# Kernel optimization log

Measured on AMD Instinct MI355X. Metric: run time of the kernel, lower is better.

Reference implementation:

```python
import jax, jax.numpy as jnp
import numpy as np

DN = ('NCHW', 'OIHW', 'NCHW')


def conv(x, w, s, p):
    return jax.lax.conv_general_dilated(x, w, (s, s), [(p, p), (p, p)], dimension_numbers=DN)


def batchnorm(x, g, b, eps=1e-5):
    # torch BatchNorm2d in training mode: biased batch stats over (N,H,W)
    mu = jnp.mean(x, (0, 2, 3), keepdims=True)
    var = jnp.var(x, (0, 2, 3), keepdims=True)
    return (x - mu) * jax.lax.rsqrt(var + eps) * g.reshape(1, -1, 1, 1) + b.reshape(1, -1, 1, 1)


def pconv(x, mask, W, b, s, p, gb, act):
    # PartialConvLayer.forward
    k = W.shape[-1]
    y = conv(x * mask, W, s, p)
    mc = conv(mask, jnp.ones((1, 1, k, k), x.dtype), s, p)  # all-ones mask conv (frozen)
    zero = mc == 0
    msum = jnp.where(zero, 1.0, mc)
    if b is not None:
        bias = b.reshape(1, -1, 1, 1)
        y = (y - bias) / msum + bias
    else:
        y = y / msum
    y = jnp.where(zero, 0.0, y)
    new_mask = jnp.where(zero, 0.0, 1.0).astype(x.dtype)
    if gb is not None:
        y = batchnorm(y, gb[0], gb[1])
    if act == 'relu':
        y = jax.nn.relu(y)
    elif act == 'leaky':
        y = jnp.where(y >= 0, y, 0.2 * y)
    return y, new_mask


def nlm(mask, feat, h2):
    # Vectorized batch_NLM: Nadaraya-Watson estimator between miss and bkg pixels.
    # Equivalent to the original triple loop: for each miss pixel i,
    #   out[i] = sum_j exp(-||x_i-x_j||^2/h^2) x_j / sum_j exp(-...)   over bkg j.
    # Subtracting the per-row min distance before exp is mathematically identical
    # (the factor cancels in the ratio) and numerically stable.
    bs, C, H, W = feat.shape
    N = H * W
    x = feat.transpose(0, 2, 3, 1).reshape(bs, N, C)
    bkg = mask.reshape(bs, N) > 0.5
    sq = jnp.sum(x * x, -1)  # [bs,N]
    D = jnp.maximum(sq[:, :, None] + sq[:, None, :] - 2.0 * jnp.einsum('bic,bjc->bij', x, x), 0.0)
    Dm = jnp.where(bkg[:, None, :], D, jnp.inf)
    dmin = jnp.min(Dm, -1, keepdims=True)
    w = jnp.where(bkg[:, None, :], jnp.exp(-(D - dmin) / h2), 0.0)
    avg = jnp.einsum('bij,bjc->bic', w, x) / jnp.sum(w, -1, keepdims=True)
    out = jnp.where(bkg[:, :, None], x, avg)  # only miss pixels are replaced
    return out.reshape(bs, H, W, C).transpose(0, 3, 1, 2)


def up2(x):
    return jnp.repeat(jnp.repeat(x, 2, axis=2), 2, axis=3)


def forward(input_x, mask, enc1_W, enc2_W, enc3_W, enc4_W, dec4_W, dec3_W, dec2_W, dec1_W, dec1_b,
            enc2_g, enc2_b, enc3_g, enc3_b, enc4_g, enc4_b,
            dec4_g, dec4_b, dec3_g, dec3_b, dec2_g, dec2_b):
    H_GAUSS2 = 25.0  # h_gaussian = 5
    h0, m0 = input_x, mask
    h1, m1 = pconv(h0, m0, enc1_W, None, 2, 3, None, 'relu')                 # down-7, bn=False
    h2, m2 = pconv(h1, m1, enc2_W, None, 2, 2, (enc2_g, enc2_b), 'relu')     # down-5
    # NLM feature swapping at layer 2 (torch code detaches -> stop_gradient)
    h2 = jax.lax.stop_gradient(nlm(m2, h2, H_GAUSS2))
    buffer_swapped = h2
    h3, m3 = pconv(h2, m2, enc3_W, None, 2, 1, (enc3_g, enc3_b), 'relu')     # down-3
    h4, m4 = pconv(h3, m3, enc4_W, None, 2, 1, (enc4_g, enc4_b), 'relu')     # down-3

    out, omask = h4, m4
    out, omask = up2(out), up2(omask)
    out, omask = pconv(jnp.concatenate([out, h3], 1), omask, dec4_W, None, 1, 1, (dec4_g, dec4_b), 'leaky')
    out, omask = up2(out), up2(omask)
    out, omask = pconv(jnp.concatenate([out, buffer_swapped], 1), omask, dec3_W, None, 1, 1, (dec3_g, dec3_b), 'leaky')
    out, omask = up2(out), up2(omask)
    out, omask = pconv(jnp.concatenate([out, h1], 1), omask, dec2_W, None, 1, 1, (dec2_g, dec2_b), 'leaky')
    out, omask = up2(out), up2(omask)
    out, omask = pconv(jnp.concatenate([out, h0], 1), omask, dec1_W, dec1_b, 1, 1, None, 'none')  # bn=False, bias, no act
    return out


def setup_inputs() -> dict:
    key = jax.random.key(0)
    ks = jax.random.split(key, 12)

    def kaiming(k, shape):
        fan_in = shape[1] * shape[2] * shape[3]
        return jax.random.normal(k, shape, jnp.float32) * np.float32(np.sqrt(2.0 / fan_in))

    bs = 8
    input_x = jax.random.normal(ks[0], (bs, 128, 144, 144), jnp.float32)
    # mask: 1 = background (valid), 0 = missing. Hole large enough to survive two downsamples.
    mask = jnp.ones((bs, 1, 144, 144), jnp.float32).at[:, :, 40:96, 40:96].set(0.0)

    inp = {
        'input_x': input_x,
        'mask': mask,
        'enc1_W': kaiming(ks[1], (256, 128, 7, 7)),
        'enc2_W': kaiming(ks[2], (512, 256, 5, 5)),
        'enc3_W': kaiming(ks[3], (512, 512, 3, 3)),
        'enc4_W': kaiming(ks[4], (512, 512, 3, 3)),
        'dec4_W': kaiming(ks[5], (512, 1024, 3, 3)),
        'dec3_W': kaiming(ks[6], (512, 1024, 3, 3)),
        'dec2_W': kaiming(ks[7], (256, 768, 3, 3)),
        'dec1_W': kaiming(ks[8], (128, 384, 3, 3)),
        'dec1_b': jnp.zeros((128,), jnp.float32),
    }
    for name, c in [('enc2', 512), ('enc3', 512), ('enc4', 512), ('dec4', 512), ('dec3', 512), ('dec2', 256)]:
        inp[name + '_g'] = jnp.ones((c,), jnp.float32)
        inp[name + '_b'] = jnp.zeros((c,), jnp.float32)
    return inp


def reference(input_x, mask, enc1_W, enc2_W, enc3_W, enc4_W, dec4_W, dec3_W, dec2_W, dec1_W, dec1_b,
              enc2_g, enc2_b, enc3_g, enc3_b, enc4_g, enc4_b,
              dec4_g, dec4_b, dec3_g, dec3_b, dec2_g, dec2_b):
    return forward(input_x, mask, enc1_W, enc2_W, enc3_W, enc4_W, dec4_W, dec3_W, dec2_W, dec1_W, dec1_b,
                   enc2_g, enc2_b, enc3_g, enc3_b, enc4_g, enc4_b,
                   dec4_g, dec4_b, dec3_g, dec3_b, dec2_g, dec2_b)
```

## Files before the change

### kernel.cpp

```cpp
#include <hip/hip_runtime.h>
#include <math.h>

#define ACT_NONE 0
#define ACT_RELU 1
#define ACT_LEAKY 2

#define EPI_F32 0
#define EPI_PAIR_RELU 1
#define EPI_F32_BIAS 2

typedef __attribute__((ext_vector_type(8))) short short8;
typedef __attribute__((ext_vector_type(8))) __bf16 bf16x8;
typedef __attribute__((ext_vector_type(4))) float f32x4;
typedef __attribute__((ext_vector_type(4))) unsigned uint4v;

__device__ __forceinline__ float actf(float y, int act) {
    if (act == ACT_RELU)  return y > 0.f ? y : 0.f;
    if (act == ACT_LEAKY) return y >= 0.f ? y : 0.2f * y;
    return y;
}

__device__ __forceinline__ unsigned f2bf_rne(float f) {
    unsigned u = __float_as_uint(f);
    return (u + 0x7FFFu + ((u >> 16) & 1u)) >> 16;
}
__device__ __forceinline__ float bf2f(unsigned h) { return __uint_as_float(h << 16); }
__device__ __forceinline__ unsigned splitpack(float f) {
    unsigned hi = f2bf_rne(f);
    float r = f - bf2f(hi);
    unsigned lo = f2bf_rne(r);
    return (hi & 0xFFFFu) | (lo << 16);
}

__device__ __forceinline__ f32x4 mfma16(short8 a, short8 b, f32x4 c) {
    return __builtin_amdgcn_mfma_f32_16x16x32_bf16(
        __builtin_bit_cast(bf16x8, a), __builtin_bit_cast(bf16x8, b), c, 0, 0, 0);
}

__device__ __forceinline__ size_t paddr(int img, int KBc, size_t HW, size_t pix) {
    return ((size_t)img * KBc * HW + pix) * 32;
}

template<int K, int S, bool MHALF>
__global__ void maskconv_kernel(const float* __restrict__ M, int HM, int WM,
                                float* __restrict__ mc, float* __restrict__ nm,
                                int N, int Hin, int Win, int Hout, int Wout) {
    constexpr int P = (K - 1) / 2;
    int idx = blockIdx.x * blockDim.x + threadIdx.x;
    int total = N * Hout * Wout;
    if (idx >= total) return;
    int wo = idx % Wout;
    int t  = idx / Wout;
    int ho = t % Hout;
    int n  = t / Hout;
    float s = 0.f;
    for (int kh = 0; kh < K; ++kh) {
        int ih = ho * S - P + kh;
        if ((unsigned)ih >= (unsigned)Hin) continue;
        const float* mrow = M + ((size_t)n * HM + (MHALF ? (ih >> 1) : ih)) * WM;
        for (int kw = 0; kw < K; ++kw) {
            int iw = wo * S - P + kw;
            if ((unsigned)iw < (unsigned)Win)
                s += mrow[MHALF ? (iw >> 1) : iw];
        }
    }
    mc[idx] = s;
    nm[idx] = (s == 0.f) ? 0.f : 1.f;
}

__global__ void wtransform(const float* __restrict__ W, short* __restrict__ Whi,
                           short* __restrict__ Wlo, int Cout, int Cin, int Ksz,
                           size_t total) {
    size_t idx = (size_t)blockIdx.x * blockDim.x + threadIdx.x;
    if (idx >= total) return;
    int j = (int)(idx & 7);
    int lane = (int)((idx >> 3) & 63);
    size_t r = idx >> 9;
    int COB = Cout >> 4, KB = Cin >> 5;
    int cob = (int)(r % COB); r /= COB;
    int kb = (int)(r % KB);
    int tap = (int)(r / KB);
    int co = cob * 16 + (lane & 15);
    int ci = kb * 32 + (lane >> 4) * 8 + j;
    float f = W[((size_t)co * Cin + ci) * Ksz + tap];
    unsigned hi = f2bf_rne(f);
    float rr = f - bf2f(hi);
    unsigned lo = f2bf_rne(rr);
    Whi[idx] = (short)hi;
    Wlo[idx] = (short)lo;
}

template<int K, int S, int TH, int TW, int NFW, bool AF32, int EPI>
__global__ __launch_bounds__(512) void conv_enc(
    const void* __restrict__ Ahi, const void* __restrict__ Alo,
    int Cin, int Hin, int Win,
    const float* __restrict__ M,
    const short* __restrict__ Whi, const short* __restrict__ Wlo,
    const float* __restrict__ mc, const float* __restrict__ bias,
    void* __restrict__ outp, void* __restrict__ outp2,
    int Hout, int Wout, int Cout, int TX)
{
    static_assert(S == 2, "parity layout assumes stride 2");
    constexpr int P = (K - 1) / 2;
    constexpr int HH  = (TH - 1) * S + K;
    constexpr int HWC = (TW - 1) * S + K;
    constexpr int PXC = HH * HWC;
    static_assert(PXC <= 512, "one halo pixel per thread");
    constexpr int PW  = (HWC + 1) / 2;
    constexpr int PXC2 = HH * PW * 2;
    constexpr int PXC2P = PXC2 + ((2 - (PXC2 % 8) + 8) % 8);
    __shared__ __align__(16) short BHs[4 * PXC2P * 8];
    __shared__ __align__(16) short BLs[4 * PXC2P * 8];

    const int t    = threadIdx.x;
    const int lane = t & 63;
    const int wv   = t >> 6;
    const int wm   = wv >> 1;
    const int wn   = wv & 1;
    const int img  = blockIdx.z;
    const int coB  = blockIdx.y * 256;
    const int tile = blockIdx.x;
    const int ty   = tile / TX, tx = tile - ty * TX;
    const int oy0  = ty * TH, ox0 = tx * TW;
    const int KB   = Cin >> 5;
    const int COB  = Cout >> 4;
    const size_t HW = (size_t)Hin * Win;
    const int g  = lane >> 4;
    const int pl = lane & 15;

    bool sel = false;
    size_t basef = 0, basep = 0;
    int qq = 0;
    if (t < PXC) {
        const int r = t / HWC, c = t - r * HWC;
        qq = r * PW + (c >> 1) + (c & 1) * (HH * PW);
        const int iy = oy0 * S - P + r;
        const int ix = ox0 * S - P + c;
        if ((unsigned)iy < (unsigned)Hin && (unsigned)ix < (unsigned)Win) {
            const size_t pix = (size_t)iy * Win + ix;
            if (M[(size_t)img * HW + pix] != 0.f) {
                sel = true;
                basef = (size_t)img * Cin * HW + pix;
                basep = paddr(img, KB, HW, pix);
            }
        }
    }

    short8 hv[4], lv[4];
    auto prefetch = [&](int kb) {
#pragma unroll
        for (int gg = 0; gg < 4; ++gg) {
            if (sel) {
                if (AF32) {
                    const float* s = (const float*)Ahi + basef + (size_t)(kb * 32 + gg * 8) * HW;
#pragma unroll
                    for (int j = 0; j < 8; ++j) {
                        float f = s[(size_t)j * HW];
                        unsigned h16 = f2bf_rne(f);
                        float rr = f - bf2f(h16);
                        hv[gg][j] = (short)h16;
                        lv[gg][j] = (short)f2bf_rne(rr);
                    }
                } else {
                    const size_t a = basep + (size_t)kb * HW * 32 + gg * 8;
                    hv[gg] = *(const short8*)((const short*)Ahi + a);
                    lv[gg] = *(const short8*)((const short*)Alo + a);
                }
            } else {
#pragma unroll
                for (int j = 0; j < 8; ++j) { hv[gg][j] = 0; lv[gg][j] = 0; }
            }
        }
    };

    f32x4 acc[4][NFW] = {};
    if (t < PXC) prefetch(0);

#pragma unroll 1
    for (int kb = 0; kb < KB; ++kb) {
        if (t < PXC) {
#pragma unroll
            for (int gg = 0; gg < 4; ++gg) {
                *(short8*)&BHs[(gg * PXC2P + qq) * 8] = hv[gg];
                *(short8*)&BLs[(gg * PXC2P + qq) * 8] = lv[gg];
            }
        }
        __syncthreads();
        if (t < PXC && kb + 1 < KB) prefetch(kb + 1);

#pragma unroll 1
        for (int kh = 0; kh < K; ++kh)
#pragma unroll 1
        for (int kw = 0; kw < K; ++kw) {
            const int tap = kh * K + kw;
            const size_t wb = (((size_t)tap * KB + kb) * COB + (coB >> 4) + wm * 4) * 512
                            + (size_t)lane * 8;
            short8 ah[4], al[4];
#pragma unroll
            for (int fm = 0; fm < 4; ++fm) {
                ah[fm] = *(const short8*)(Whi + wb + (size_t)fm * 512);
                al[fm] = *(const short8*)(Wlo + wb + (size_t)fm * 512);
            }
#pragma unroll
            for (int fn = 0; fn < NFW; ++fn) {
                const int pxf = (wn * NFW + fn) * 16 + pl;
                const int oy = pxf / TW, ox = pxf - oy * TW;
                const int q2 = (oy * S + kh) * PW + ox + (kw >> 1) + (kw & 1) * (HH * PW);
                short8 bh = *(const short8*)&BHs[(g * PXC2P + q2) * 8];
                short8 bl = *(const short8*)&BLs[(g * PXC2P + q2) * 8];
#pragma unroll
                for (int fm = 0; fm < 4; ++fm) {
                    acc[fm][fn] = mfma16(ah[fm], bh, acc[fm][fn]);
                    acc[fm][fn] = mfma16(al[fm], bh, acc[fm][fn]);
                    acc[fm][fn] = mfma16(ah[fm], bl, acc[fm][fn]);
                }
            }
        }
        __syncthreads();
    }

    const int Npix = Hout * Wout;
    const float* mcb = mc + (size_t)img * Npix;
#pragma unroll
    for (int fm = 0; fm < 4; ++fm)
#pragma unroll
    for (int fn = 0; fn < NFW; ++fn) {
        const int co = coB + (wm * 4 + fm) * 16 + (lane >> 4) * 4;
        const int pxf = (wn * NFW + fn) * 16 + (lane & 15);
        const int oy = pxf / TW, ox = pxf - oy * TW;
        const int gy = oy0 + oy, gx = ox0 + ox;
        if (gy >= Hout || gx >= Wout) continue;
        const size_t pix = (size_t)gy * Wout + gx;
        const float m = mcb[pix];
        f32x4 a = acc[fm][fn];
#pragma unroll
        for (int r = 0; r < 4; ++r) {
            float y = a[r];
            if (EPI == EPI_F32_BIAS) {
                const float bv = bias[co + r];
                y = (m == 0.f) ? 0.f : (y - bv) / m + bv;
            } else {
                y = (m == 0.f) ? 0.f : y / m;
            }
            if (EPI == EPI_PAIR_RELU) {
                y = y > 0.f ? y : 0.f;
                const size_t pa = paddr(img, Cout >> 5, Npix, pix)
                                + (size_t)(co >> 5) * Npix * 32 + (co & 31) + r;
                unsigned h16 = f2bf_rne(y);
                float rr = y - bf2f(h16);
                ((short*)outp)[pa]  = (short)h16;
                ((short*)outp2)[pa] = (short)f2bf_rne(rr);
            } else {
                ((float*)outp)[((size_t)img * Cout + co + r) * Npix + pix] = y;
            }
        }
    }
}

template<int TH, int TW, int NFW, bool BF32, int EPI>
__global__ __launch_bounds__(512) void conv3x3(
    const void* __restrict__ Ahi, const void* __restrict__ Alo,
    int CA, int HA, int WA,
    const void* __restrict__ Bhi, const void* __restrict__ Blo, int CB,
    const float* __restrict__ M,
    const short* __restrict__ Whi, const short* __restrict__ Wlo,
    const float* __restrict__ mc, const float* __restrict__ bias,
    void* __restrict__ outp,
    int Hout, int Wout, int Cout, int TX)
{
    constexpr int HALO_H = TH + 2, HALO_W = TW + 2, HALO = HALO_H * HALO_W;
    constexpr int HALOP = HALO + ((2 - (HALO % 8) + 8) % 8);
    constexpr int NPIX = TH * TW;
    constexpr int SITER = (HALO + 127) / 128;
    static_assert(NPIX == 32 * NFW, "tile must be exactly 32*NFW pixels");
    __shared__ __align__(16) short BHs[4 * HALOP * 8];
    __shared__ __align__(16) short BLs[4 * HALOP * 8];

    const int t    = threadIdx.x;
    const int lane = t & 63;
    const int wv   = t >> 6;
    const int wm   = wv >> 1;
    const int wn   = wv & 1;
    const int img  = blockIdx.z;
    const int coB  = blockIdx.y * 128;
    const int tile = blockIdx.x;
    const int ty   = tile / TX;
    const int tx   = tile - ty * TX;
    const int oy0  = ty * TH, ox0 = tx * TW;
    const int Cin  = CA + CB;
    const int KB   = Cin >> 5;
    const int KBA  = CA >> 5;
    const int KBB  = CB >> 5;
    const int COB  = Cout >> 4;
    const int WM   = Wout >> 1;
    const size_t HWA = (size_t)HA * WA;
    const size_t HWB = (size_t)Hout * Wout;

    const int sg = t >> 7;
    const int st = t & 127;
    const int g  = lane >> 4;
    const int pl = lane & 15;

    bool ssel[SITER];
    size_t aoff[SITER], boff[SITER];
#pragma unroll
    for (int i = 0; i < SITER; ++i) {
        ssel[i] = false; aoff[i] = 0; boff[i] = 0;
        const int q = st + i * 128;
        if (q < HALO) {
            const int hy = q / HALO_W, hx = q - hy * HALO_W;
            const int iy = oy0 - 1 + hy, ix = ox0 - 1 + hx;
            if ((unsigned)iy < (unsigned)Hout && (unsigned)ix < (unsigned)Wout) {
                if (M[((size_t)img * (Hout >> 1) + (iy >> 1)) * WM + (ix >> 1)] != 0.f) {
                    ssel[i] = true;
                    const size_t pixA = (size_t)(iy >> 1) * WA + (ix >> 1);
                    const size_t pixB = (size_t)iy * Wout + ix;
                    aoff[i] = paddr(img, KBA, HWA, pixA) + sg * 8;
                    if (BF32) boff[i] = (size_t)img * CB * HWB + pixB;
                    else      boff[i] = paddr(img, KBB, HWB, pixB) + sg * 8;
                }
            }
        }
    }

    short8 hv[SITER], lv[SITER];
    auto prefetch = [&](int kb) {
        const int c = kb * 32 + sg * 8;
#pragma unroll
        for (int i = 0; i < SITER; ++i) {
            const int q = st + i * 128;
            bool ok = (q < HALO) && ssel[i];
            if (ok) {
                if (c < CA) {
                    const size_t a = aoff[i] + (size_t)kb * HWA * 32;
                    hv[i] = *(const short8*)((const short*)Ahi + a);
                    lv[i] = *(const short8*)((const short*)Alo + a);
                } else {
                    if (BF32) {
                        const float* s = (const float*)Bhi + boff[i] + (size_t)(c - CA) * HWB;
#pragma unroll
                        for (int j = 0; j < 8; ++j) {
                            float f = s[(size_t)j * HWB];
                            unsigned h16 = f2bf_rne(f);
                            float rr = f - bf2f(h16);
                            hv[i][j] = (short)h16;
                            lv[i][j] = (short)f2bf_rne(rr);
                        }
                    } else {
                        const size_t a = boff[i] + (size_t)(kb - KBA) * HWB * 32;
                        hv[i] = *(const short8*)((const short*)Bhi + a);
                        lv[i] = *(const short8*)((const short*)Blo + a);
                    }
                }
            } else {
#pragma unroll
                for (int j = 0; j < 8; ++j) { hv[i][j] = 0; lv[i][j] = 0; }
            }
        }
    };

    f32x4 acc[2][NFW] = {};
    const size_t wstride = (size_t)KB * COB * 512;
    prefetch(0);

#pragma unroll 1
    for (int kb = 0; kb < KB; ++kb) {
#pragma unroll
        for (int i = 0; i < SITER; ++i) {
            const int q = st + i * 128;
            if (q < HALO) {
                *(short8*)&BHs[(sg * HALOP + q) * 8] = hv[i];
                *(short8*)&BLs[(sg * HALOP + q) * 8] = lv[i];
            }
        }
        __syncthreads();
        if (kb + 1 < KB) prefetch(kb + 1);

        size_t wb = ((size_t)kb * COB + (coB >> 4) + wm * 2) * 512 + lane * 8;
#pragma unroll 1
        for (int tap = 0; tap < 9; ++tap) {
            const int dh = tap / 3, dw = tap - dh * 3;
            short8 ah0 = *(const short8*)(Whi + wb);
            short8 ah1 = *(const short8*)(Whi + wb + 512);
            short8 al0 = *(const short8*)(Wlo + wb);
            short8 al1 = *(const short8*)(Wlo + wb + 512);
#pragma unroll
            for (int fn = 0; fn < NFW; ++fn) {
                const int pxf = (wn * NFW + fn) * 16 + pl;
                const int oy = pxf / TW, ox = pxf - oy * TW;
                const int hpx = (oy + dh) * HALO_W + (ox + dw);
                short8 bh = *(const short8*)&BHs[(g * HALOP + hpx) * 8];
                short8 bl = *(const short8*)&BLs[(g * HALOP + hpx) * 8];
                acc[0][fn] = mfma16(ah0, bh, acc[0][fn]);
                acc[1][fn] = mfma16(ah1, bh, acc[1][fn]);
                acc[0][fn] = mfma16(al0, bh, acc[0][fn]);
                acc[1][fn] = mfma16(al1, bh, acc[1][fn]);
                acc[0][fn] = mfma16(ah0, bl, acc[0][fn]);
                acc[1][fn] = mfma16(ah1, bl, acc[1][fn]);
            }
            wb += wstride;
        }
        __syncthreads();
    }

    const float* mcb = mc + (size_t)img * HWB;
#pragma unroll
    for (int fm = 0; fm < 2; ++fm)
#pragma unroll
    for (int fn = 0; fn < NFW; ++fn) {
        const int co = coB + (wm * 2 + fm) * 16 + (lane >> 4) * 4;
        const int pxf = (wn * NFW + fn) * 16 + (lane & 15);
        const int oy = pxf / TW, ox = pxf - oy * TW;
        const int gy = oy0 + oy, gx = ox0 + ox;
        if (gy >= Hout || gx >= Wout) continue;
        const float m = mcb[(size_t)gy * Wout + gx];
        f32x4 a = acc[fm][fn];
#pragma unroll
        for (int r = 0; r < 4; ++r) {
            float y = a[r];
            if (EPI == EPI_F32_BIAS) {
                const float bv = bias[co + r];
                y = (m == 0.f) ? 0.f : (y - bv) / m + bv;
            } else {
                y = (m == 0.f) ? 0.f : y / m;
            }
            ((float*)outp)[((size_t)img * Cout + co + r) * HWB + (size_t)gy * Wout + gx] = y;
        }
    }
}

__global__ __launch_bounds__(256) void bn_stats_kernel(const float* __restrict__ y,
                                                       int N, int C, int HW,
                                                       float* __restrict__ mean,
                                                       float* __restrict__ istd) {
    const int c = blockIdx.x;
    double s = 0.0, s2 = 0.0;
    const int tot = N * HW;
    for (int i = threadIdx.x; i < tot; i += blockDim.x) {
        int n = i / HW, hw = i - n * HW;
        float v = y[((size_t)n * C + c) * HW + hw];
        s += v;
        s2 += (double)v * v;
    }
    __shared__ double sh[256], sh2[256];
    sh[threadIdx.x] = s; sh2[threadIdx.x] = s2;
    __syncthreads();
    for (int o = 128; o > 0; o >>= 1) {
        if (threadIdx.x < o) { sh[threadIdx.x] += sh[threadIdx.x + o]; sh2[threadIdx.x] += sh2[threadIdx.x + o]; }
        __syncthreads();
    }
    if (threadIdx.x == 0) {
        double mu = sh[0] / tot;
        double var = sh2[0] / tot - mu * mu;
        mean[c] = (float)mu;
        istd[c] = (float)(1.0 / sqrt(var + 1e-5));
    }
}

__global__ __launch_bounds__(256) void bn_apply_blk(
    const float* __restrict__ y,
    const float* __restrict__ mean, const float* __restrict__ istd,
    const float* __restrict__ g, const float* __restrict__ b,
    short* __restrict__ hi, short* __restrict__ lo, float* __restrict__ fout,
    int C, int HW, int act) {
    __shared__ float tile[32][65];
    const int img = blockIdx.z, kb = blockIdx.y;
    const int px0 = blockIdx.x * 64;
    const int tid = threadIdx.x;
    const int KBc = C >> 5;

    for (int i = tid; i < 32 * 64; i += 256) {
        const int ch = i >> 6, px = i & 63;
        float v = 0.f;
        if (px0 + px < HW)
            v = y[((size_t)img * C + kb * 32 + ch) * HW + px0 + px];
        tile[ch][px] = v;
    }
    __syncthreads();

    const int px = tid >> 2, sg = tid & 3;
    if (px0 + px < HW) {
        short8 h8, l8;
        float f8[8];
#pragma unroll
        for (int j = 0; j < 8; ++j) {
            const int c = kb * 32 + sg * 8 + j;
            float v = tile[sg * 8 + j][px];
            v = (v - mean[c]) * istd[c] * g[c] + b[c];
            v = actf(v, act);
            f8[j] = v;
            unsigned h16 = f2bf_rne(v);
            float rr = v - bf2f(h16);
            h8[j] = (short)h16;
            l8[j] = (short)f2bf_rne(rr);
        }
        const size_t a = (((size_t)img * KBc + kb) * HW + px0 + px) * 32 + sg * 8;
        *(short8*)&hi[a] = h8;
        *(short8*)&lo[a] = l8;
        if (fout) {
#pragma unroll
            for (int j = 0; j < 8; ++j)
                fout[((size_t)img * C + kb * 32 + sg * 8 + j) * HW + px0 + px] = f8[j];
        }
    }
}

#define NLM_C 512
#define NLM_N 1296
#define NLM_MAXM 256
#define NLM_RT 16
#define NLM_KB1 16
#define NLM_KB2 41
#define NLM_PFRAG (NLM_KB1 * NLM_RT * 512)
#define NLM_WFRAG (NLM_KB2 * NLM_RT * 512)

__global__ __launch_bounds__(256) void nlm_trans(const float* __restrict__ h2f,
                                                 unsigned* __restrict__ xTp) {
    __shared__ float tile[32][33];
    const int b = blockIdx.z;
    const int j0 = blockIdx.x * 32, c0 = blockIdx.y * 32;
    const int tx = threadIdx.x & 31, ty = threadIdx.x >> 5;
    for (int cc = ty; cc < 32; cc += 8) {
        const int j = j0 + tx;
        tile[cc][tx] = (j < NLM_N) ? h2f[((size_t)b * NLM_C + c0 + cc) * NLM_N + j] : 0.f;
    }
    __syncthreads();
    for (int jj = ty; jj < 32; jj += 8) {
        const int j = j0 + jj;
        if (j < NLM_N)
            xTp[((size_t)b * NLM_N + j) * NLM_C + c0 + tx] = splitpack(tile[tx][jj]);
    }
}

__global__ void nlm_sq2(const float* __restrict__ h2f, float* __restrict__ sq) {
    const int b = blockIdx.y;
    const int j = blockIdx.x * 256 + threadIdx.x;
    if (j >= NLM_N) return;
    const float* p = h2f + (size_t)b * NLM_C * NLM_N + j;
    float s0 = 0.f, s1 = 0.f, s2 = 0.f, s3 = 0.f;
    for (int c = 0; c < NLM_C; c += 4) {
        float v0 = p[(size_t)c * NLM_N];
        float v1 = p[(size_t)(c + 1) * NLM_N];
        float v2 = p[(size_t)(c + 2) * NLM_N];
        float v3 = p[(size_t)(c + 3) * NLM_N];
        s0 = fmaf(v0, v0, s0); s1 = fmaf(v1, v1, s1);
        s2 = fmaf(v2, v2, s2); s3 = fmaf(v3, v3, s3);
    }
    sq[b * NLM_N + j] = (s0 + s1) + (s2 + s3);
}

__global__ void nlm_compact(const float* __restrict__ nm2, int* __restrict__ list,
                            int* __restrict__ cnt) {
    const int b = blockIdx.x;
    for (int j = threadIdx.x; j < NLM_N; j += 256) {
        if (nm2[(size_t)b * NLM_N + j] == 0.f) {
            int pos = atomicAdd(&cnt[b], 1);
            if (pos < NLM_MAXM) list[b * NLM_MAXM + pos] = j;
        }
    }
}

__global__ void nlm_gather(const unsigned* __restrict__ xTp, const int* __restrict__ list,
                           const int* __restrict__ cnt,
                           short* __restrict__ Phi, short* __restrict__ Plo) {
    const int b = blockIdx.y;
    const int id = blockIdx.x * 256 + threadIdx.x;
    const int i  = id >> 6;
    const int rem = id & 63;
    const int kb = rem >> 2, kg = rem & 3;
    const int lane = kg * 16 + (i & 15), rt = i >> 4;
    const size_t f = (size_t)b * NLM_PFRAG + ((size_t)(kb * NLM_RT + rt) * 64 + lane) * 8;
    if (i < cnt[b]) {
        const int pix = list[b * NLM_MAXM + i];
        const unsigned* s = xTp + ((size_t)b * NLM_N + pix) * NLM_C + kb * 32 + kg * 8;
#pragma unroll
        for (int jj = 0; jj < 8; ++jj) {
            unsigned v = s[jj];
            Phi[f + jj] = (short)(v & 0xFFFFu);
            Plo[f + jj] = (short)(v >> 16);
        }
    } else {
#pragma unroll
        for (int jj = 0; jj < 8; ++jj) { Phi[f + jj] = 0; Plo[f + jj] = 0; }
    }
}

__global__ __launch_bounds__(512) void nlm_gemm1(
    const unsigned* __restrict__ xTp, const short* __restrict__ Phi,
    const short* __restrict__ Plo, const int* __restrict__ cnt,
    float* __restrict__ S) {
    const int img = blockIdx.z, mt = blockIdx.y, nt = blockIdx.x;
    if (mt * 128 >= cnt[img]) return;
    __shared__ __align__(16) unsigned BH[4 * 128 * 4];
    __shared__ __align__(16) unsigned BL[4 * 128 * 4];
    const int t = threadIdx.x, lane = t & 63, wv = t >> 6, wm = wv >> 1, wn = wv & 1;
    const int j0 = nt * 128;
    const int spx = t & 127, sg = t >> 7;
    f32x4 acc[2][4] = {};
#pragma unroll 1
    for (int kb = 0; kb < NLM_KB1; ++kb) {
        unsigned v[8];
#pragma unroll
        for (int jj = 0; jj < 8; ++jj) v[jj] = 0u;
        const int j = j0 + spx;
        if (j < NLM_N) {
            const unsigned* s = xTp + ((size_t)img * NLM_N + j) * NLM_C + kb * 32 + sg * 8;
#pragma unroll
            for (int jj = 0; jj < 8; ++jj) v[jj] = s[jj];
        }
        uint4v hd, ld;
#pragma unroll
        for (int jj = 0; jj < 4; ++jj) {
            hd[jj] = (v[2 * jj] & 0xFFFFu) | (v[2 * jj + 1] << 16);
            ld[jj] = (v[2 * jj] >> 16) | (v[2 * jj + 1] & 0xFFFF0000u);
        }
        *(uint4v*)&BH[(sg * 128 + spx) * 4] = hd;
        *(uint4v*)&BL[(sg * 128 + spx) * 4] = ld;
        __syncthreads();
        const size_t ab = (size_t)img * NLM_PFRAG
                        + (size_t)(kb * NLM_RT + mt * 8 + wm * 2) * 512 + (size_t)lane * 8;
        short8 ah0 = *(const short8*)(Phi + ab);
        short8 ah1 = *(const short8*)(Phi + ab + 512);
        short8 al0 = *(const short8*)(Plo + ab);
        short8 al1 = *(const short8*)(Plo + ab + 512);
        const int g = lane >> 4, pl = lane & 15;
#pragma unroll
        for (int fn = 0; fn < 4; ++fn) {
            const int px = wn * 64 + fn * 16 + pl;
            short8 bh = *(const short8*)&BH[(g * 128 + px) * 4];
            short8 bl = *(const short8*)&BL[(g * 128 + px) * 4];
            acc[0][fn] = mfma16(ah0, bh, acc[0][fn]);
            acc[1][fn] = mfma16(ah1, bh, acc[1][fn]);
            acc[0][fn] = mfma16(al0, bh, acc[0][fn]);
            acc[1][fn] = mfma16(al1, bh, acc[1][fn]);
            acc[0][fn] = mfma16(ah0, bl, acc[0][fn]);
            acc[1][fn] = mfma16(ah1, bl, acc[1][fn]);
        }
        __syncthreads();
    }
#pragma unroll
    for (int fm = 0; fm < 2; ++fm)
#pragma unroll
    for (int fn = 0; fn < 4; ++fn) {
        const int row = mt * 128 + (wm * 2 + fm) * 16 + (lane >> 4) * 4;
        const int j = j0 + wn * 64 + fn * 16 + (lane & 15);
        if (j >= NLM_N) continue;
        f32x4 a = acc[fm][fn];
#pragma unroll
        for (int r = 0; r < 4; ++r)
            S[((size_t)img * NLM_MAXM + row + r) * NLM_N + j] = a[r];
    }
}

__global__ __launch_bounds__(256) void nlm_row(
    const float* __restrict__ S, const float* __restrict__ sq,
    const float* __restrict__ nm2, const int* __restrict__ list,
    const int* __restrict__ cnt,
    short* __restrict__ W2hi, short* __restrict__ W2lo,
    float* __restrict__ sumw, float inv_h2) {
    const int img = blockIdx.y, i = blockIdx.x;
    if (i >= cnt[img] || i >= NLM_MAXM) return;
    __shared__ float Drow[NLM_N];
    __shared__ float red[256];
    const int tid = threadIdx.x;
    const int pix = list[img * NLM_MAXM + i];
    const float sqi = sq[img * NLM_N + pix];
    const float BIG = 3.4e38f;
    float lmin = BIG;
    for (int j = tid; j < NLM_N; j += 256) {
        float d = BIG;
        if (nm2[(size_t)img * NLM_N + j] != 0.f) {
            float dot = S[((size_t)img * NLM_MAXM + i) * NLM_N + j];
            d = sqi + sq[img * NLM_N + j] - 2.f * dot;
            d = d > 0.f ? d : 0.f;
            lmin = d < lmin ? d : lmin;
        }
        Drow[j] = d;
    }
    red[tid] = lmin;
    __syncthreads();
    for (int o = 128; o > 0; o >>= 1) {
        if (tid < o) red[tid] = fminf(red[tid], red[tid + o]);
        __syncthreads();
    }
    const float dmin = red[0];
    __syncthreads();

    const int rt = i >> 4, lr = i & 15;
    float lsum = 0.f;
    for (int j = tid; j < NLM_KB2 * 32; j += 256) {
        float w = 0.f;
        if (j < NLM_N && Drow[j] < 3.3e38f) {
            w = expf(-(Drow[j] - dmin) * inv_h2);
            lsum += w;
        }
        const unsigned u = splitpack(w);
        const int kb = j >> 5, kg = (j & 31) >> 3, jj = j & 7;
        const int lane = kg * 16 + lr;
        const size_t f = (size_t)img * NLM_WFRAG
                       + ((size_t)(kb * NLM_RT + rt) * 64 + lane) * 8 + jj;
        W2hi[f] = (short)(u & 0xFFFFu);
        W2lo[f] = (short)(u >> 16);
    }
    red[tid] = lsum;
    __syncthreads();
    for (int o = 128; o > 0; o >>= 1) {
        if (tid < o) red[tid] += red[tid + o];
        __syncthreads();
    }
    if (tid == 0) sumw[img * NLM_MAXM + i] = red[0];
}

__global__ __launch_bounds__(512) void nlm_gemm2(
    const unsigned* __restrict__ xTp, const short* __restrict__ W2hi,
    const short* __restrict__ W2lo, const int* __restrict__ cnt,
    const float* __restrict__ sumw, const int* __restrict__ list,
    short* __restrict__ outHi, short* __restrict__ outLo) {
    const int img = blockIdx.z, mt = blockIdx.y, ct = blockIdx.x;
    const int cN = cnt[img] < NLM_MAXM ? cnt[img] : NLM_MAXM;
    if (mt * 128 >= cN) return;
    __shared__ __align__(16) unsigned BH[4 * 128 * 4];
    __shared__ __align__(16) unsigned BL[4 * 128 * 4];
    const int t = threadIdx.x, lane = t & 63, wv = t >> 6, wm = wv >> 1, wn = wv & 1;
    const int c0 = ct * 128;
    const int sc = t & 127, sg = t >> 7;
    f32x4 acc[2][4] = {};
#pragma unroll 1
    for (int kb = 0; kb < NLM_KB2; ++kb) {
        unsigned v[8];
#pragma unroll
        for (int jj = 0; jj < 8; ++jj) {
            const int j = kb * 32 + sg * 8 + jj;
            v[jj] = (j < NLM_N)
                  ? xTp[((size_t)img * NLM_N + j) * NLM_C + c0 + sc] : 0u;
        }
        uint4v hd, ld;
#pragma unroll
        for (int jj = 0; jj < 4; ++jj) {
            hd[jj] = (v[2 * jj] & 0xFFFFu) | (v[2 * jj + 1] << 16);
            ld[jj] = (v[2 * jj] >> 16) | (v[2 * jj + 1] & 0xFFFF0000u);
        }
        *(uint4v*)&BH[(sg * 128 + sc) * 4] = hd;
        *(uint4v*)&BL[(sg * 128 + sc) * 4] = ld;
        __syncthreads();
        const size_t ab = (size_t)img * NLM_WFRAG
                        + (size_t)(kb * NLM_RT + mt * 8 + wm * 2) * 512 + (size_t)lane * 8;
        short8 ah0 = *(const short8*)(W2hi + ab);
        short8 ah1 = *(const short8*)(W2hi + ab + 512);
        short8 al0 = *(const short8*)(W2lo + ab);
        short8 al1 = *(const short8*)(W2lo + ab + 512);
        const int g = lane >> 4, pl = lane & 15;
#pragma unroll
        for (int fn = 0; fn < 4; ++fn) {
            const int px = wn * 64 + fn * 16 + pl;
            short8 bh = *(const short8*)&BH[(g * 128 + px) * 4];
            short8 bl = *(const short8*)&BL[(g * 128 + px) * 4];
            acc[0][fn] = mfma16(ah0, bh, acc[0][fn]);
            acc[1][fn] = mfma16(ah1, bh, acc[1][fn]);
            acc[0][fn] = mfma16(al0, bh, acc[0][fn]);
            acc[1][fn] = mfma16(al1, bh, acc[1][fn]);
            acc[0][fn] = mfma16(ah0, bl, acc[0][fn]);
            acc[1][fn] = mfma16(ah1, bl, acc[1][fn]);
        }
        __syncthreads();
    }
#pragma unroll
    for (int fm = 0; fm < 2; ++fm)
#pragma unroll
    for (int fn = 0; fn < 4; ++fn) {
        const int row = mt * 128 + (wm * 2 + fm) * 16 + (lane >> 4) * 4;
        const int c = c0 + wn * 64 + fn * 16 + (lane & 15);
        f32x4 a = acc[fm][fn];
#pragma unroll
        for (int r = 0; r < 4; ++r) {
            const int ri = row + r;
            if (ri < cN) {
                const float y = a[r] / sumw[img * NLM_MAXM + ri];
                const int pix = list[img * NLM_MAXM + ri];
                const size_t pa = (((size_t)img * (NLM_C >> 5) + (c >> 5)) * NLM_N + pix) * 32
                                + (c & 31);
                unsigned h16 = f2bf_rne(y);
                float rr = y - bf2f(h16);
                outHi[pa] = (short)h16;
                outLo[pa] = (short)f2bf_rne(rr);
            }
        }
    }
}

extern "C" void kernel_launch(void* const* d_in, const int* in_sizes, int n_in,
                              void* d_out, int out_size, void* d_ws, size_t ws_size,
                              hipStream_t stream) {
    const float* x0    = (const float*)d_in[0];
    const float* m0    = (const float*)d_in[1];
    const float* Wsrc[8] = {
        (const float*)d_in[2], (const float*)d_in[3], (const float*)d_in[4],
        (const float*)d_in[5], (const float*)d_in[6], (const float*)d_in[7],
        (const float*)d_in[8], (const float*)d_in[9]
    };
    const float* dec1b = (const float*)d_in[10];
    const float* enc2g = (const float*)d_in[11];
    const float* enc2b = (const float*)d_in[12];
    const float* enc3g = (const float*)d_in[13];
    const float* enc3b = (const float*)d_in[14];
    const float* enc4g = (const float*)d_in[15];
    const float* enc4b = (const float*)d_in[16];
    const float* dec4g = (const float*)d_in[17];
    const float* dec4b = (const float*)d_in[18];
    const float* dec3g = (const float*)d_in[19];
    const float* dec3b = (const float*)d_in[20];
    const float* dec2g = (const float*)d_in[21];
    const float* dec2b = (const float*)d_in[22];
    float* outp = (float*)d_out;

    const int N = 8;
    float* ws = (float*)d_ws;
    size_t off = 0;
    auto alloc = [&](size_t nf) {
        size_t o = off;
        off += ((nf + 63) / 64) * 64;
        return ws + o;
    };
    auto allocPair = [&](size_t E, short** hi, short** lo) {
        float* p = alloc(E);
        *hi = (short*)p;
        *lo = (short*)p + E;
    };

    short *h1hi, *h1lo, *h2shi, *h2slo, *h3hi, *h3lo, *h4hi, *h4lo, *d4hi, *d4lo;
    allocPair(10616832, &h1hi, &h1lo);
    allocPair(5308416, &h2shi, &h2slo);
    allocPair(1327104, &h3hi, &h3lo);
    allocPair(331776, &h4hi, &h4lo);
    allocPair(1327104, &d4hi, &d4lo);
    float* ybuf = alloc(10616832);
    float* h2f  = alloc(5308416);
    unsigned* xTp = (unsigned*)alloc(5308416);
    float* sqb  = alloc(10368);
    float* mc   = alloc(165888);
    float* nm1  = alloc(41472);
    float* nm2  = alloc(10368);
    float* nm3  = alloc(2592);
    float* nm4  = alloc(648);
    float* nmd4 = alloc(2592);
    float* nmd3 = alloc(10368);
    float* nmd2 = alloc(41472);
    float* nmx  = alloc(165888);
    float* bmean = alloc(512);
    float* bistd = alloc(512);
    short* Whi = (short*)alloc(10625024);
    short* Wlo = (short*)alloc(10625024);
    float* Smat = alloc((size_t)8 * NLM_MAXM * NLM_N);
    float* Phi_  = alloc((size_t)8 * NLM_PFRAG / 2);
    float* Plo_  = alloc((size_t)8 * NLM_PFRAG / 2);
    float* W2hi_ = alloc((size_t)8 * NLM_WFRAG / 2);
    float* W2lo_ = alloc((size_t)8 * NLM_WFRAG / 2);
    short* Phi = (short*)Phi_;  short* Plo = (short*)Plo_;
    short* W2hi = (short*)W2hi_; short* W2lo = (short*)W2lo_;
    int*   mlist = (int*)alloc(8 * NLM_MAXM);
    int*   mcnt  = (int*)alloc(64);
    float* sumw  = alloc(8 * NLM_MAXM);
    short* d3hi = h2shi; short* d3lo = h2slo;
    short* d2hi = h1hi;  short* d2lo = h1lo;

    if (ws_size < off * sizeof(float)) return;

    auto cdiv = [](size_t a, size_t b) { return (int)((a + b - 1) / b); };

    struct WLay { int Cout, Cin, K; size_t ofs; };
    const WLay WL[8] = {
        {256, 128, 7, 0},
        {512, 256, 5, 1605632},
        {512, 512, 3, 4882432},
        {512, 512, 3, 7241728},
        {512, 1024, 3, 9601024},
        {512, 1024, 3, 14319616},
        {256, 768, 3, 19038208},
        {128, 384, 3, 20807680},
    };
    for (int i = 0; i < 8; ++i) {
        size_t tot = (size_t)WL[i].Cout * WL[i].Cin * WL[i].K * WL[i].K;
        wtransform<<<cdiv(tot, 256), 256, 0, stream>>>(
            Wsrc[i], Whi + WL[i].ofs, Wlo + WL[i].ofs, WL[i].Cout, WL[i].Cin,
            WL[i].K * WL[i].K, tot);
    }

    maskconv_kernel<7, 2, false><<<cdiv(N * 72 * 72, 256), 256, 0, stream>>>(
        m0, 144, 144, mc, nm1, N, 144, 144, 72, 72);
    conv_enc<7, 2, 8, 8, 2, true, EPI_PAIR_RELU><<<dim3(81, 1, N), 512, 0, stream>>>(
        x0, nullptr, 128, 144, 144, m0,
        Whi + WL[0].ofs, Wlo + WL[0].ofs, mc, nullptr, h1hi, h1lo,
        72, 72, 256, 9);

    maskconv_kernel<5, 2, false><<<cdiv(N * 36 * 36, 256), 256, 0, stream>>>(
        nm1, 72, 72, mc, nm2, N, 72, 72, 36, 36);
    conv_enc<5, 2, 8, 8, 2, false, EPI_F32><<<dim3(25, 2, N), 512, 0, stream>>>(
        h1hi, h1lo, 256, 72, 72, nm1,
        Whi + WL[1].ofs, Wlo + WL[1].ofs, mc, nullptr, ybuf, nullptr,
        36, 36, 512, 5);
    bn_stats_kernel<<<512, 256, 0, stream>>>(ybuf, N, 512, 1296, bmean, bistd);
    bn_apply_blk<<<dim3(cdiv(1296, 64), 16, N), 256, 0, stream>>>(
        ybuf, bmean, bistd, enc2g, enc2b, h2shi, h2slo, h2f, 512, 1296, ACT_RELU);

    nlm_trans<<<dim3(41, 16, N), 256, 0, stream>>>(h2f, xTp);
    nlm_sq2<<<dim3(6, N), 256, 0, stream>>>(h2f, sqb);
    hipMemsetAsync(mcnt, 0, 8 * sizeof(int), stream);
    nlm_compact<<<N, 256, 0, stream>>>(nm2, mlist, mcnt);
    nlm_gather<<<dim3(64, N), 256, 0, stream>>>(xTp, mlist, mcnt, Phi, Plo);
    nlm_gemm1<<<dim3(11, 2, N), 512, 0, stream>>>(xTp, Phi, Plo, mcnt, Smat);
    nlm_row<<<dim3(NLM_MAXM, N), 256, 0, stream>>>(Smat, sqb, nm2, mlist, mcnt,
                                                   W2hi, W2lo, sumw, 1.f / 25.f);
    nlm_gemm2<<<dim3(4, 2, N), 512, 0, stream>>>(xTp, W2hi, W2lo, mcnt, sumw,
                                                 mlist, h2shi, h2slo);

    maskconv_kernel<3, 2, false><<<cdiv(N * 18 * 18, 256), 256, 0, stream>>>(
        nm2, 36, 36, mc, nm3, N, 36, 36, 18, 18);
    conv_enc<3, 2, 4, 8, 1, false, EPI_F32><<<dim3(15, 2, N), 512, 0, stream>>>(
        h2shi, h2slo, 512, 36, 36, nm2,
        Whi + WL[2].ofs, Wlo + WL[2].ofs, mc, nullptr, ybuf, nullptr,
        18, 18, 512, 3);
    bn_stats_kernel<<<512, 256, 0, stream>>>(ybuf, N, 512, 324, bmean, bistd);
    bn_apply_blk<<<dim3(cdiv(324, 64), 16, N), 256, 0, stream>>>(
        ybuf, bmean, bistd, enc3g, enc3b, h3hi, h3lo, nullptr, 512, 324, ACT_RELU);

    maskconv_kernel<3, 2, false><<<cdiv(N * 9 * 9, 256), 256, 0, stream>>>(
        nm3, 18, 18, mc, nm4, N, 18, 18, 9, 9);
    conv_enc<3, 2, 4, 8, 1, false, EPI_F32><<<dim3(6, 2, N), 512, 0, stream>>>(
        h3hi, h3lo, 512, 18, 18, nm3,
        Whi + WL[3].ofs, Wlo + WL[3].ofs, mc, nullptr, ybuf, nullptr,
        9, 9, 512, 2);
    bn_stats_kernel<<<512, 256, 0, stream>>>(ybuf, N, 512, 81, bmean, bistd);
    bn_apply_blk<<<dim3(cdiv(81, 64), 16, N), 256, 0, stream>>>(
        ybuf, bmean, bistd, enc4g, enc4b, h4hi, h4lo, nullptr, 512, 81, ACT_RELU);

    maskconv_kernel<3, 1, true><<<cdiv(N * 18 * 18, 256), 256, 0, stream>>>(
        nm4, 9, 9, mc, nmd4, N, 18, 18, 18, 18);
    conv3x3<8, 8, 2, false, EPI_F32><<<dim3(9, 4, N), 512, 0, stream>>>(
        h4hi, h4lo, 512, 9, 9, h3hi, h3lo, 512, nm4,
        Whi + WL[4].ofs, Wlo + WL[4].ofs, mc, nullptr, ybuf,
        18, 18, 512, 3);
    bn_stats_kernel<<<512, 256, 0, stream>>>(ybuf, N, 512, 324, bmean, bistd);
    bn_apply_blk<<<dim3(cdiv(324, 64), 16, N), 256, 0, stream>>>(
        ybuf, bmean, bistd, dec4g, dec4b, d4hi, d4lo, nullptr, 512, 324, ACT_LEAKY);

    maskconv_kernel<3, 1, true><<<cdiv(N * 36 * 36, 256), 256, 0, stream>>>(
        nmd4, 18, 18, mc, nmd3, N, 36, 36, 36, 36);
    conv3x3<8, 12, 3, false, EPI_F32><<<dim3(15, 4, N), 512, 0, stream>>>(
        d4hi, d4lo, 512, 18, 18, h2shi, h2slo, 512, nmd4,
        Whi + WL[5].ofs, Wlo + WL[5].ofs, mc, nullptr, ybuf,
        36, 36, 512, 3);
    bn_stats_kernel<<<512, 256, 0, stream>>>(ybuf, N, 512, 1296, bmean, bistd);
    bn_apply_blk<<<dim3(cdiv(1296, 64), 16, N), 256, 0, stream>>>(
        ybuf, bmean, bistd, dec3g, dec3b, d3hi, d3lo, nullptr, 512, 1296, ACT_LEAKY);

    maskconv_kernel<3, 1, true><<<cdiv(N * 72 * 72, 256), 256, 0, stream>>>(
        nmd3, 36, 36, mc, nmd2, N, 72, 72, 72, 72);
    conv3x3<8, 16, 4, false, EPI_F32><<<dim3(45, 2, N), 512, 0, stream>>>(
        d3hi, d3lo, 512, 36, 36, h1hi, h1lo, 256, nmd3,
        Whi + WL[6].ofs, Wlo + WL[6].ofs, mc, nullptr, ybuf,
        72, 72, 256, 5);
    bn_stats_kernel<<<256, 256, 0, stream>>>(ybuf, N, 256, 5184, bmean, bistd);
    bn_apply_blk<<<dim3(cdiv(5184, 64), 8, N), 256, 0, stream>>>(
        ybuf, bmean, bistd, dec2g, dec2b, d2hi, d2lo, nullptr, 256, 5184, ACT_LEAKY);

    maskconv_kernel<3, 1, true><<<cdiv(N * 144 * 144, 256), 256, 0, stream>>>(
        nmd2, 72, 72, mc, nmx, N, 144, 144, 144, 144);
    conv3x3<8, 16, 4, true, EPI_F32_BIAS><<<dim3(162, 1, N), 512, 0, stream>>>(
        d2hi, d2lo, 256, 72, 72, x0, nullptr, 128, nmd2,
        Whi + WL[7].ofs, Wlo + WL[7].ofs, mc, dec1b, outp,
        144, 144, 128, 9);
}
```

Baseline: 2.780 ms.

## Add specialized enc1 conv with pre-split bf16 input planes and larger tiles

Adds a pre-pass that converts the fp32 NCHW input into channel-blocked hi/lo bf16 planes, stored in the output buffer as scratch. A dedicated 7x7 stride-2 enc1 kernel then tiles 8x16 output pixels by 128 output channels. The halo is staged in LDS in parity-split layout, and the fused ReLU epilogue writes split bf16 outputs. This removes per-tile fp32 conversion and improves reuse of staged inputs across channels. The cost is an extra pass over the input and reuse of the output buffer as scratch.

```diff
diff --git a/kernel.cpp b/kernel.cpp
--- a/kernel.cpp
+++ b/kernel.cpp
@@ -88,6 +88,177 @@
     unsigned lo = f2bf_rne(rr);
     Whi[idx] = (short)hi;
     Wlo[idx] = (short)lo;
+}
+
+__global__ __launch_bounds__(256) void split_planes(
+    const float* __restrict__ x, short* __restrict__ hi, short* __restrict__ lo,
+    int C, int HW) {
+    __shared__ float tile[32][65];
+    const int img = blockIdx.z, kb = blockIdx.y;
+    const int px0 = blockIdx.x * 64;
+    const int tid = threadIdx.x;
+    const int KBc = C >> 5;
+    for (int i = tid; i < 32 * 64; i += 256) {
+        const int ch = i >> 6, px = i & 63;
+        float v = 0.f;
+        if (px0 + px < HW)
+            v = x[((size_t)img * C + kb * 32 + ch) * HW + px0 + px];
+        tile[ch][px] = v;
+    }
+    __syncthreads();
+    const int px = tid >> 2, sg = tid & 3;
+    if (px0 + px < HW) {
+        short8 h8, l8;
+#pragma unroll
+        for (int j = 0; j < 8; ++j) {
+            float v = tile[sg * 8 + j][px];
+            unsigned h16 = f2bf_rne(v);
+            float rr = v - bf2f(h16);
+            h8[j] = (short)h16;
+            l8[j] = (short)f2bf_rne(rr);
+        }
+        const size_t a = (((size_t)img * KBc + kb) * HW + px0 + px) * 32 + sg * 8;
+        *(short8*)&hi[a] = h8;
+        *(short8*)&lo[a] = l8;
+    }
+}
+
+#define E1_HH 21
+#define E1_HWC 37
+#define E1_PXC 777
+#define E1_PW 19
+#define E1_PXC2P 802
+#define E1_PLANE (4 * E1_PXC2P * 8)
+#define E1_LDS_BYTES (2 * E1_PLANE * 2)
+
+__global__ __launch_bounds__(512) void conv_enc1(
+    const short* __restrict__ Ahi, const short* __restrict__ Alo,
+    const float* __restrict__ M,
+    const short* __restrict__ Whi, const short* __restrict__ Wlo,
+    const float* __restrict__ mc,
+    short* __restrict__ outHi, short* __restrict__ outLo)
+{
+    extern __shared__ short smem[];
+    short* BHs = smem;
+    short* BLs = smem + E1_PLANE;
+
+    constexpr int Cin = 128, Cout = 256, Hin = 144, Win = 144, Hout = 72, Wout = 72;
+    constexpr int KB = 4, COB = 16, NFW = 4;
+    const int t = threadIdx.x;
+    const int lane = t & 63;
+    const int wv = t >> 6;
+    const int wm = wv >> 1;
+    const int wn = wv & 1;
+    const int img = blockIdx.z;
+    const int coB = blockIdx.y * 128;
+    const int tile = blockIdx.x;
+    const int ty = tile / 5, tx = tile - ty * 5;
+    const int oy0 = ty * 8, ox0 = tx * 16;
+    const size_t HW = (size_t)Hin * Win;
+    const int g = lane >> 4, pl = lane & 15;
+
+    bool sel[2]; size_t basep[2]; int qq[2];
+#pragma unroll
+    for (int i = 0; i < 2; ++i) {
+        sel[i] = false; basep[i] = 0; qq[i] = 0;
+        const int q = t + i * 512;
+        if (q < E1_PXC) {
+            const int r = q / E1_HWC, c = q - r * E1_HWC;
+            qq[i] = r * E1_PW + (c >> 1) + (c & 1) * (E1_HH * E1_PW);
+            const int iy = oy0 * 2 - 3 + r;
+            const int ix = ox0 * 2 - 3 + c;
+            if ((unsigned)iy < (unsigned)Hin && (unsigned)ix < (unsigned)Win) {
+                const size_t pix = (size_t)iy * Win + ix;
+                if (M[(size_t)img * HW + pix] != 0.f) {
+                    sel[i] = true;
+                    basep[i] = paddr(img, KB, HW, pix);
+                }
+            }
+        }
+    }
+
+    f32x4 acc[2][NFW] = {};
+
+#pragma unroll 1
+    for (int kb = 0; kb < KB; ++kb) {
+#pragma unroll
+        for (int i = 0; i < 2; ++i) {
+            const int q = t + i * 512;
+            if (q < E1_PXC) {
+#pragma unroll
+                for (int gg = 0; gg < 4; ++gg) {
+                    short8 h8, l8;
+                    if (sel[i]) {
+                        const size_t a = basep[i] + (size_t)kb * HW * 32 + gg * 8;
+                        h8 = *(const short8*)(Ahi + a);
+                        l8 = *(const short8*)(Alo + a);
+                    } else {
+#pragma unroll
+                        for (int j = 0; j < 8; ++j) { h8[j] = 0; l8[j] = 0; }
+                    }
+                    *(short8*)&BHs[((size_t)gg * E1_PXC2P + qq[i]) * 8] = h8;
+                    *(short8*)&BLs[((size_t)gg * E1_PXC2P + qq[i]) * 8] = l8;
+                }
+            }
+        }
+        __syncthreads();
+
+#pragma unroll 1
+        for (int kh = 0; kh < 7; ++kh)
+#pragma unroll 1
+        for (int kw = 0; kw < 7; ++kw) {
+            const int tap = kh * 7 + kw;
+            const size_t wb = (((size_t)tap * KB + kb) * COB + (coB >> 4) + wm * 2) * 512
+                            + (size_t)lane * 8;
+            short8 ah0 = *(const short8*)(Whi + wb);
+            short8 ah1 = *(const short8*)(Whi + wb + 512);
+            short8 al0 = *(const short8*)(Wlo + wb);
+            short8 al1 = *(const short8*)(Wlo + wb + 512);
+#pragma unroll
+            for (int fn = 0; fn < NFW; ++fn) {
+                const int pxf = (wn * NFW + fn) * 16 + pl;
+                const int oy = pxf >> 4, ox = pxf & 15;
+                const int q2 = (oy * 2 + kh) * E1_PW + ox + (kw >> 1)
+                             + (kw & 1) * (E1_HH * E1_PW);
+                short8 bh = *(const short8*)&BHs[((size_t)g * E1_PXC2P + q2) * 8];
+                short8 bl = *(const short8*)&BLs[((size_t)g * E1_PXC2P + q2) * 8];
+                acc[0][fn] = mfma16(ah0, bh, acc[0][fn]);
+                acc[1][fn] = mfma16(ah1, bh, acc[1][fn]);
+                acc[0][fn] = mfma16(al0, bh, acc[0][fn]);
+                acc[1][fn] = mfma16(al1, bh, acc[1][fn]);
+                acc[0][fn] = mfma16(ah0, bl, acc[0][fn]);
+                acc[1][fn] = mfma16(ah1, bl, acc[1][fn]);
+            }
+        }
+        __syncthreads();
+    }
+
+    constexpr int Npix = Hout * Wout;
+    const float* mcb = mc + (size_t)img * Npix;
+#pragma unroll
+    for (int fm = 0; fm < 2; ++fm)
+#pragma unroll
+    for (int fn = 0; fn < NFW; ++fn) {
+        const int co = coB + (wm * 2 + fm) * 16 + (lane >> 4) * 4;
+        const int pxf = (wn * NFW + fn) * 16 + (lane & 15);
+        const int oy = pxf >> 4, ox = pxf & 15;
+        const int gy = oy0 + oy, gx = ox0 + ox;
+        if (gy >= Hout || gx >= Wout) continue;
+        const size_t pix = (size_t)gy * Wout + gx;
+        const float m = mcb[pix];
+        f32x4 a = acc[fm][fn];
+#pragma unroll
+        for (int r = 0; r < 4; ++r) {
+            float y = (m == 0.f) ? 0.f : a[r] / m;
+            y = y > 0.f ? y : 0.f;
+            const size_t pa = paddr(img, Cout >> 5, Npix, pix)
+                            + (size_t)((co + r) >> 5) * Npix * 32 + ((co + r) & 31);
+            unsigned h16 = f2bf_rne(y);
+            float rr = y - bf2f(h16);
+            outHi[pa] = (short)h16;
+            outLo[pa] = (short)f2bf_rne(rr);
+        }
+    }
 }
 
 template<int K, int S, int TH, int TW, int NFW, bool AF32, int EPI>
@@ -885,12 +1056,16 @@
             WL[i].K * WL[i].K, tot);
     }
 
+    short* x0hi = (short*)d_out;
+    short* x0lo = x0hi + 21233664;
+    split_planes<<<dim3(324, 4, N), 256, 0, stream>>>(x0, x0hi, x0lo, 128, 20736);
+
     maskconv_kernel<7, 2, false><<<cdiv(N * 72 * 72, 256), 256, 0, stream>>>(
         m0, 144, 144, mc, nm1, N, 144, 144, 72, 72);
-    conv_enc<7, 2, 8, 8, 2, true, EPI_PAIR_RELU><<<dim3(81, 1, N), 512, 0, stream>>>(
-        x0, nullptr, 128, 144, 144, m0,
-        Whi + WL[0].ofs, Wlo + WL[0].ofs, mc, nullptr, h1hi, h1lo,
-        72, 72, 256, 9);
+    (void)hipFuncSetAttribute((const void*)conv_enc1,
+                              hipFuncAttributeMaxDynamicSharedMemorySize, E1_LDS_BYTES);
+    conv_enc1<<<dim3(45, 2, N), 512, E1_LDS_BYTES, stream>>>(
+        x0hi, x0lo, m0, Whi + WL[0].ofs, Wlo + WL[0].ofs, mc, h1hi, h1lo);
 
     maskconv_kernel<5, 2, false><<<cdiv(N * 36 * 36, 256), 256, 0, stream>>>(
         nm1, 72, 72, mc, nm2, N, 72, 72, 36, 36);
```

After: 2.810 ms. Within noise of the previous version (+1.1%).

## Pre-split enc1 input into bf16 hi/lo planes and raise MFMA wave priority

Applied to the files above, without the earlier changes.

Adds a transpose kernel that converts the fp32 NCHW input into channel-blocked bf16 hi/lo planes, written into scratch space in the output buffer. The first encoder conv then reads these planes directly instead of converting fp32 inside its halo loads. Separately, s_setprio is raised around the MFMA inner loops in both conv kernels so waves issuing matrix ops get scheduling priority. The cost is an extra kernel launch and an extra pass over the input, and the output buffer is used as scratch, which is only safe if it is large enough and written later.

```diff
diff --git a/kernel.cpp b/kernel.cpp
--- a/kernel.cpp
+++ b/kernel.cpp
@@ -90,6 +90,39 @@
     Wlo[idx] = (short)lo;
 }
 
+__global__ __launch_bounds__(256) void split_planes(
+    const float* __restrict__ x, short* __restrict__ hi, short* __restrict__ lo,
+    int C, int HW) {
+    __shared__ float tile[32][65];
+    const int img = blockIdx.z, kb = blockIdx.y;
+    const int px0 = blockIdx.x * 64;
+    const int tid = threadIdx.x;
+    const int KBc = C >> 5;
+    for (int i = tid; i < 32 * 64; i += 256) {
+        const int ch = i >> 6, px = i & 63;
+        float v = 0.f;
+        if (px0 + px < HW)
+            v = x[((size_t)img * C + kb * 32 + ch) * HW + px0 + px];
+        tile[ch][px] = v;
+    }
+    __syncthreads();
+    const int px = tid >> 2, sg = tid & 3;
+    if (px0 + px < HW) {
+        short8 h8, l8;
+#pragma unroll
+        for (int j = 0; j < 8; ++j) {
+            float v = tile[sg * 8 + j][px];
+            unsigned h16 = f2bf_rne(v);
+            float rr = v - bf2f(h16);
+            h8[j] = (short)h16;
+            l8[j] = (short)f2bf_rne(rr);
+        }
+        const size_t a = (((size_t)img * KBc + kb) * HW + px0 + px) * 32 + sg * 8;
+        *(short8*)&hi[a] = h8;
+        *(short8*)&lo[a] = l8;
+    }
+}
+
 template<int K, int S, int TH, int TW, int NFW, bool AF32, int EPI>
 __global__ __launch_bounds__(512) void conv_enc(
     const void* __restrict__ Ahi, const void* __restrict__ Alo,
@@ -201,6 +234,7 @@
                 ah[fm] = *(const short8*)(Whi + wb + (size_t)fm * 512);
                 al[fm] = *(const short8*)(Wlo + wb + (size_t)fm * 512);
             }
+            __builtin_amdgcn_s_setprio(1);
 #pragma unroll
             for (int fn = 0; fn < NFW; ++fn) {
                 const int pxf = (wn * NFW + fn) * 16 + pl;
@@ -215,6 +249,7 @@
                     acc[fm][fn] = mfma16(ah[fm], bl, acc[fm][fn]);
                 }
             }
+            __builtin_amdgcn_s_setprio(0);
         }
         __syncthreads();
     }
@@ -384,6 +419,7 @@
             short8 ah1 = *(const short8*)(Whi + wb + 512);
             short8 al0 = *(const short8*)(Wlo + wb);
             short8 al1 = *(const short8*)(Wlo + wb + 512);
+            __builtin_amdgcn_s_setprio(1);
 #pragma unroll
             for (int fn = 0; fn < NFW; ++fn) {
                 const int pxf = (wn * NFW + fn) * 16 + pl;
@@ -398,6 +434,7 @@
                 acc[0][fn] = mfma16(ah0, bl, acc[0][fn]);
                 acc[1][fn] = mfma16(ah1, bl, acc[1][fn]);
             }
+            __builtin_amdgcn_s_setprio(0);
             wb += wstride;
         }
         __syncthreads();
@@ -885,10 +922,14 @@
             WL[i].K * WL[i].K, tot);
     }
 
+    short* x0hi = (short*)d_out;
+    short* x0lo = x0hi + 21233664;
+    split_planes<<<dim3(324, 4, N), 256, 0, stream>>>(x0, x0hi, x0lo, 128, 20736);
+
     maskconv_kernel<7, 2, false><<<cdiv(N * 72 * 72, 256), 256, 0, stream>>>(
         m0, 144, 144, mc, nm1, N, 144, 144, 72, 72);
-    conv_enc<7, 2, 8, 8, 2, true, EPI_PAIR_RELU><<<dim3(81, 1, N), 512, 0, stream>>>(
-        x0, nullptr, 128, 144, 144, m0,
+    conv_enc<7, 2, 8, 8, 2, false, EPI_PAIR_RELU><<<dim3(81, 1, N), 512, 0, stream>>>(
+        x0hi, x0lo, 128, 144, 144, m0,
         Whi + WL[0].ofs, Wlo + WL[0].ofs, mc, nullptr, h1hi, h1lo,
         72, 72, 256, 9);
 
```

Result: no change. 2.757 ms (median of 3 runs) (-0.8%).
